# Performance work log

Hardware: AMD Instinct MI355X
Metric: run time of the kernel (lower is better)

## Reference

```python
import jax, jax.numpy as jnp
import numpy as np

N, L, H, D = 4, 1024, 8, 64

def setup_inputs() -> dict:
    key = jax.random.key(0)
    ks = jax.random.split(key, 6)
    names = ["q_real", "q_imag", "k_real", "k_imag", "v_real", "v_imag"]
    return {n: jax.random.normal(k, (N, L, H, D), dtype=jnp.float32) for n, k in zip(names, ks)}


def reference(q_real, q_imag, k_real, k_imag, v_real, v_imag):
    d = q_real.shape[-1]
    scale = 1.0 / np.sqrt(d).astype(np.float32)
    # complex QK^T: (ar+i*ai)(br+i*bi) -> 4 real einsums, scores shape (N,H,L,S)
    s_real = (jnp.einsum('nlhd,nshd->nhls', q_real, k_real)
              - jnp.einsum('nlhd,nshd->nhls', q_imag, k_imag))
    s_imag = (jnp.einsum('nlhd,nshd->nhls', q_real, k_imag)
              + jnp.einsum('nlhd,nshd->nhls', q_imag, k_real))
    # complex softmax = independent softmax on real and imag parts
    w_real = jax.nn.softmax(scale * s_real, axis=-1)
    w_imag = jax.nn.softmax(scale * s_imag, axis=-1)
    # complex_dropout on complex input is identity (original code drops nothing)
    # complex AV
    u_real = (jnp.einsum('nhls,nshd->nlhd', w_real, v_real)
              - jnp.einsum('nhls,nshd->nlhd', w_imag, v_imag))
    u_imag = (jnp.einsum('nhls,nshd->nlhd', w_real, v_imag)
              + jnp.einsum('nhls,nshd->nlhd', w_imag, v_real))
    # attn_weights.permute(0,2,1,3).mean(dim=-2): (N,H,L,S)->(N,L,H,S), mean over H -> (N,L,S)
    a_real = w_real.mean(axis=1)
    a_imag = w_imag.mean(axis=1)
    return (u_real, u_imag, a_real, a_imag)
```

## Files before the change

kernel.cpp:

```cpp
#include <hip/hip_runtime.h>

#define N_ 4
#define L_ 1024
#define H_ 8
#define D_ 64

typedef _Float16 f16x8 __attribute__((ext_vector_type(8)));
typedef _Float16 f16x4 __attribute__((ext_vector_type(4)));
typedef _Float16 f16x2 __attribute__((ext_vector_type(2)));
typedef float f32x4 __attribute__((ext_vector_type(4)));

#define MFMA(A, B, C) __builtin_amdgcn_mfma_f32_16x16x32_f16(A, B, C, 0, 0, 0)
#define EXP2(x) __builtin_amdgcn_exp2f(x)

__device__ __forceinline__ ushort f2h(float x) {
    union { _Float16 h; ushort u; } c;
    c.h = (_Float16)x;
    return c.u;
}
__device__ __forceinline__ f16x8 ld8(const ushort* p) {
    return *(const f16x8*)p;
}
__device__ __forceinline__ f16x4 pack4(float a, float b, float c, float d) {
    union { f16x4 v; f16x2 h[2]; } u;
    u.h[0] = __builtin_bit_cast(f16x2, __builtin_amdgcn_cvt_pkrtz(a, b));
    u.h[1] = __builtin_bit_cast(f16x2, __builtin_amdgcn_cvt_pkrtz(c, d));
    return u.v;
}
__device__ __forceinline__ f16x8 negf(f16x8 a) {
    uint4 u = __builtin_bit_cast(uint4, a);
    u.x ^= 0x80008000u; u.y ^= 0x80008000u; u.z ^= 0x80008000u; u.w ^= 0x80008000u;
    return __builtin_bit_cast(f16x8, u);
}
__device__ __forceinline__ f16x8 cvt8s(const float* p, float s) {
    float4 a = *(const float4*)p;
    float4 b = *(const float4*)(p + 4);
    union { f16x8 v; _Float16 e[8]; } u;
    u.e[0] = (_Float16)(a.x * s); u.e[1] = (_Float16)(a.y * s);
    u.e[2] = (_Float16)(a.z * s); u.e[3] = (_Float16)(a.w * s);
    u.e[4] = (_Float16)(b.x * s); u.e[5] = (_Float16)(b.y * s);
    u.e[6] = (_Float16)(b.z * s); u.e[7] = (_Float16)(b.w * s);
    return u.v;
}
#define SCQ 0.18033688011112f
__device__ __forceinline__ f16x8 cvt8(const float* p) { return cvt8s(p, SCQ); }

__device__ __forceinline__ void gl_lds16(const ushort* g, ushort* l) {
    __builtin_amdgcn_global_load_lds(
        (const __attribute__((address_space(1))) unsigned int*)g,
        (__attribute__((address_space(3))) unsigned int*)l, 16, 0, 0);
}

__global__ void cvt_kv(const float* __restrict__ k_r, const float* __restrict__ k_i,
                       const float* __restrict__ vr, const float* __restrict__ vi,
                       ushort* __restrict__ dst) {
    __shared__ ushort t[64][72];
    const int tid = threadIdx.x;
    if (blockIdx.x < 4096) {
        int gid = blockIdx.x * 256 + tid;
        int aid = gid >> 19;
        int idx = (gid & 0x7FFFF) << 2;
        int d  = idx & 63;
        int l  = (idx >> 6) & 1023;
        int hh = (idx >> 16) & 7;
        int n  = idx >> 19;
        const float* src = aid ? k_i : k_r;
        const float4 v = *(const float4*)(src + (((long)n * 1024 + l) * 8 + hh) * 64 + d);
        ushort4 o = make_ushort4(f2h(v.x), f2h(v.y), f2h(v.z), f2h(v.w));
        *(ushort4*)(dst + ((long)aid << 21) + idx) = o;
        return;
    }
    int bid = blockIdx.x - 4096;
    int aid = bid >> 9;
    int b   = bid & 511;
    int s0  = (b & 15) << 6;
    int hh  = (b >> 4) & 7;
    int n   = b >> 7;
    const float* src = aid ? vi : vr;
    int r  = tid >> 4;
    int cq = (tid & 15) << 2;
#pragma unroll
    for (int it = 0; it < 4; ++it) {
        int s = s0 + it * 16 + r;
        const float4 v = *(const float4*)(src + (((long)n * 1024 + s) * 8 + hh) * 64 + cq);
        t[it * 16 + r][cq + 0] = f2h(v.x);
        t[it * 16 + r][cq + 1] = f2h(v.y);
        t[it * 16 + r][cq + 2] = f2h(v.z);
        t[it * 16 + r][cq + 3] = f2h(v.w);
    }
    __syncthreads();
    const int rem = cq & 31;
    const int noff = (cq & 32) + (((rem & 15) >> 2) << 3) + ((rem >> 4) << 2);
#pragma unroll
    for (int it = 0; it < 4; ++it) {
        int dd = it * 16 + r;
        ushort4 o;
        o.x = t[cq + 0][dd]; o.y = t[cq + 1][dd]; o.z = t[cq + 2][dd]; o.w = t[cq + 3][dd];
        *(ushort4*)(dst + (2l << 21) + ((long)aid << 21) +
                    (((long)n * 8 + hh) * 64 + dd) * 1024 + s0 + noff) = o;
    }
}


__launch_bounds__(512, 4)
__global__ void attn_u(const float* __restrict__ qr_g, const float* __restrict__ qi_g,
                       const ushort* __restrict__ ws, float* __restrict__ rdbuf,
                       float* __restrict__ out) {
    __shared__ ushort stgK[2][4096];
    __shared__ ushort stgV[2][4096];

    const int tid  = threadIdx.x;
    const int lane = tid & 63;
    const int wv   = tid >> 6;
    const int p    = wv >> 2;
    const int lsub = wv & 3;
    const int col  = lane & 15;
    const int g    = lane >> 4;

    const int id = blockIdx.x;
    const int x  = id & 7;
    const int j  = id >> 3;
    const int nh = x * 4 + (j >> 4);
    const int n  = nh >> 3;
    const int h  = nh & 7;
    const int l0 = (j & 15) * 64 + lsub * 16;

    const ushort* Kr = ws + ((long)nh << 16);
    const ushort* Ki = ws + (1l << 21) + ((long)nh << 16);
    const ushort* Vr = ws + (2l << 21) + ((long)nh << 16);
    const ushort* Vi = ws + (3l << 21) + ((long)nh << 16);

    const long qg = (((long)n * 1024 + l0 + col) * 8 + h) * 64 + g * 8;
    const float sgn = p ? SCQ : -SCQ;
    const f16x8 qr0 = cvt8(qr_g + qg), qr1 = cvt8(qr_g + qg + 32);
    const f16x8 qx0 = cvt8s(qi_g + qg, sgn), qx1 = cvt8s(qi_g + qg + 32, sgn);

    const int kpart = tid >> 8;
    const int ksr   = (tid >> 3) & 31;
    const int kbo   = (tid & 7) ^ (ksr & 7);
    const ushort* Ksrc = (kpart ? Ki : Kr);
    const int vd  = tid >> 3;
    const int vb  = (tid & 7) ^ (vd & 7);
    const ushort* Vsrc = ((vb >> 2) ? Vi : Vr);
    const int vbo = (vb & 3) * 8;
    ushort* kdst0 = &stgK[0][wv * 512];
    ushort* kdst1 = &stgK[1][wv * 512];
    ushort* vdst0 = &stgV[0][wv * 512];
    ushort* vdst1 = &stgV[1][wv * 512];

    float dsum = 0.f;
    f32x4 uA[4], uB[4];
#pragma unroll
    for (int db = 0; db < 4; ++db) {
        uA[db] = (f32x4){0.f, 0.f, 0.f, 0.f};
        uB[db] = (f32x4){0.f, 0.f, 0.f, 0.f};
    }

    const int kx  = (g ^ (col & 7)) * 8;
    const int kx2 = ((g + 4) ^ (col & 7)) * 8;
    const int vxA = (g ^ (col & 7)) * 8;
    const int vxB = ((4 + g) ^ (col & 7)) * 8;

#define STAGE(kd, vd_, cc)                                                   \
    do {                                                                     \
        gl_lds16(Ksrc + (long)((cc) * 32 + ksr) * 64 + kbo * 8, kd);         \
        gl_lds16(Vsrc + (long)vd * 1024 + (cc) * 32 + vbo, vd_);             \
    } while (0)

    STAGE(kdst0, vdst0, 0);
    __syncthreads();

    for (int cc = 0; cc < 32; ++cc) {
        const int buf = cc & 1;
        if (cc < 31) {
            if (buf) STAGE(kdst0, vdst0, cc + 1);
            else     STAGE(kdst1, vdst1, cc + 1);
        }
        const ushort* sk = stgK[buf];
        const ushort* sv = stgV[buf];

        union { f16x8 w8; f16x4 q[2]; } pw;
#pragma unroll
        for (int sb = 0; sb < 2; ++sb) {
            const int rb = (sb * 16 + col) * 64;
            f16x8 ka0 = ld8(&sk[p * 2048 + rb + kx]);
            f16x8 ka1 = ld8(&sk[p * 2048 + rb + kx2]);
            f16x8 kb0 = ld8(&sk[(p ^ 1) * 2048 + rb + kx]);
            f16x8 kb1 = ld8(&sk[(p ^ 1) * 2048 + rb + kx2]);
            f32x4 a0 = (f32x4){0.f, 0.f, 0.f, 0.f};
            a0 = MFMA(ka0, qr0, a0); a0 = MFMA(ka1, qr1, a0);
            a0 = MFMA(kb0, qx0, a0); a0 = MFMA(kb1, qx1, a0);
            const float w0 = EXP2(a0[0]), w1 = EXP2(a0[1]);
            const float w2 = EXP2(a0[2]), w3 = EXP2(a0[3]);
            dsum += (w0 + w1) + (w2 + w3);
            pw.q[sb] = pack4(w0, w1, w2, w3);
        }

        __builtin_amdgcn_s_setprio(1);
#pragma unroll
        for (int db = 0; db < 4; ++db) {
            const int rv = (db * 16 + col) * 64;
            uA[db] = MFMA(pw.w8, ld8(&sv[rv + vxA]), uA[db]);
            uB[db] = MFMA(pw.w8, ld8(&sv[rv + vxB]), uB[db]);
        }
        __builtin_amdgcn_s_setprio(0);

        __syncthreads();
    }

    dsum += __shfl_xor(dsum, 16);
    dsum += __shfl_xor(dsum, 32);
    const float rd = 1.f / dsum;
    if (lane < 16) rdbuf[p * 32768 + nh * 1024 + l0 + col] = rd;

    float rdl[4];
#pragma unroll
    for (int r = 0; r < 4; ++r) rdl[r] = __shfl(rd, 4 * g + r);

#pragma unroll
    for (int db = 0; db < 4; ++db) {
#pragma unroll
        for (int r = 0; r < 4; ++r) {
            uA[db][r] *= rdl[r];
            uB[db][r] *= rdl[r];
        }
    }

    float* cb = (float*)&stgK[0][0];
    const int ci = (lsub * 64 + lane) * 16;
    if (p == 1) {
#pragma unroll
        for (int db = 0; db < 4; ++db) *(f32x4*)&cb[ci + db * 4] = uB[db];
    }
    __syncthreads();
    f32x4 oR[4];
    if (p == 0) {
#pragma unroll
        for (int db = 0; db < 4; ++db) oR[db] = uA[db] - *(f32x4*)&cb[ci + db * 4];
    }
    __syncthreads();
    if (p == 1) {
#pragma unroll
        for (int db = 0; db < 4; ++db) *(f32x4*)&cb[ci + db * 4] = uA[db];
    }
    __syncthreads();

    if (p == 0) {
        const long OFF_UI = 2097152;
#pragma unroll
        for (int db = 0; db < 4; ++db) {
            f32x4 oI = uB[db] + *(f32x4*)&cb[ci + db * 4];
#pragma unroll
            for (int r = 0; r < 4; ++r) {
                const int l = l0 + 4 * g + r;
                const int d = db * 16 + col;
                const long base = (((long)n * L_ + l) * H_ + h) * D_ + d;
                out[base] = oR[db][r];
                out[OFF_UI + base] = oI[r];
            }
        }
    }
#undef STAGE
}

__launch_bounds__(256, 4)
__global__ void kern_a(const float* __restrict__ qr_g, const float* __restrict__ qi_g,
                      const ushort* __restrict__ ws, const float* __restrict__ rdbuf,
                      float* __restrict__ out) {
    __shared__ ushort stgK[2][2][64][64];
    __shared__ float lrd[8][2][64];

    const int tid  = threadIdx.x;
    const int lane = tid & 63;
    const int wv   = tid >> 6;
    const int col  = lane & 15;
    const int g    = lane >> 4;

    const int id  = blockIdx.x;
    const int x   = id & 7;
    const int q   = id >> 3;
    const int n   = x >> 1;
    const int idx = (x & 1) * 128 + q;
    const int lt0 = (idx >> 4) * 64;
    const int sc  = idx & 15;
    const int l0  = lt0 + wv * 16;

    const ushort* KrB = ws + ((long)(n * 8) << 16);
    const ushort* KiB = ws + (1l << 21) + ((long)(n * 8) << 16);

#pragma unroll
    for (int i = 0; i < 4; ++i) {
        const int t = i * 256 + tid;
        (&lrd[0][0][0])[t] =
            rdbuf[((t >> 6) & 1) * 32768 + (n * 8 + (t >> 7)) * 1024 + lt0 + (t & 63)];
    }

    const int sp   = wv >> 1;
    const int kbs  = ((lane & 7) ^ (lane >> 3)) * 8;

#define STAGEA(buf, hh)                                                      \
    do {                                                                     \
        const ushort* Kp = (sp ? KiB : KrB) + ((long)(hh) << 16);            \
        _Pragma("unroll")                                                    \
        for (int i = 0; i < 4; ++i) {                                        \
            const int krow = (wv & 1) * 32 + i * 8 + (lane >> 3);            \
            gl_lds16(Kp + (long)(sc * 64 + krow) * 64 + kbs,                 \
                     &stgK[buf][sp][(wv & 1) * 32 + i * 8][0]);              \
        }                                                                    \
    } while (0)

    f32x4 aR[4], aI[4];
#pragma unroll
    for (int i = 0; i < 4; ++i) {
        aR[i] = (f32x4){0.f, 0.f, 0.f, 0.f};
        aI[i] = (f32x4){0.f, 0.f, 0.f, 0.f};
    }

    const int kx  = (g ^ (col & 7)) * 8;
    const int kx2 = ((g + 4) ^ (col & 7)) * 8;

    STAGEA(0, 0);
    __syncthreads();

    for (int h = 0; h < 8; ++h) {
        const int buf = h & 1;
        if (h < 7) STAGEA(buf ^ 1, h + 1);

        const long qg = (((long)n * 1024 + l0 + col) * 8 + h) * 64 + g * 8;
        const f16x8 qr0 = cvt8(qr_g + qg), qr1 = cvt8(qr_g + qg + 32);
        const f16x8 qi0 = cvt8(qi_g + qg), qi1 = cvt8(qi_g + qg + 32);
        const f16x8 qn0 = negf(qi0), qn1 = negf(qi1);

        float rdR[4], rdI[4];
#pragma unroll
        for (int r = 0; r < 4; ++r) {
            rdR[r] = lrd[h][0][wv * 16 + 4 * g + r];
            rdI[r] = lrd[h][1][wv * 16 + 4 * g + r];
        }

#pragma unroll
        for (int sb = 0; sb < 4; ++sb) {
            const int row = sb * 16 + col;
            f16x8 kr0 = ld8(&stgK[buf][0][row][kx]);
            f16x8 kr1 = ld8(&stgK[buf][0][row][kx2]);
            f16x8 ki0 = ld8(&stgK[buf][1][row][kx]);
            f16x8 ki1 = ld8(&stgK[buf][1][row][kx2]);
            f32x4 a0 = (f32x4){0.f, 0.f, 0.f, 0.f};
            a0 = MFMA(qr0, kr0, a0); a0 = MFMA(qr1, kr1, a0);
            a0 = MFMA(qn0, ki0, a0); a0 = MFMA(qn1, ki1, a0);
            f32x4 a1 = (f32x4){0.f, 0.f, 0.f, 0.f};
            a1 = MFMA(qr0, ki0, a1); a1 = MFMA(qr1, ki1, a1);
            a1 = MFMA(qi0, kr0, a1); a1 = MFMA(qi1, kr1, a1);
#pragma unroll
            for (int r = 0; r < 4; ++r) {
                aR[sb][r] += EXP2(a0[r]) * rdR[r];
                aI[sb][r] += EXP2(a1[r]) * rdI[r];
            }
        }
        __syncthreads();
    }

    const long OFF_AR = 4194304;
    const long OFF_AI = 8388608;
#pragma unroll
    for (int sb = 0; sb < 4; ++sb) {
#pragma unroll
        for (int r = 0; r < 4; ++r) {
            const int l = l0 + 4 * g + r;
            const int s = sc * 64 + sb * 16 + col;
            const long ab = ((long)n * 1024 + l) * 1024 + s;
            out[OFF_AR + ab] = aR[sb][r] * 0.125f;
            out[OFF_AI + ab] = aI[sb][r] * 0.125f;
        }
    }
#undef STAGEA
}

extern "C" void kernel_launch(void* const* d_in, const int* in_sizes, int n_in,
                              void* d_out, int out_size, void* d_ws, size_t ws_size,
                              hipStream_t stream) {
    const float* qr = (const float*)d_in[0];
    const float* qi = (const float*)d_in[1];
    const float* kr = (const float*)d_in[2];
    const float* ki = (const float*)d_in[3];
    const float* vr = (const float*)d_in[4];
    const float* vi = (const float*)d_in[5];
    ushort* ws = (ushort*)d_ws;
    float* rdbuf = (float*)((char*)d_ws + (16ull << 20));
    float* out = (float*)d_out;

    hipLaunchKernelGGL(cvt_kv, dim3(5120), dim3(256), 0, stream, kr, ki, vr, vi, ws);
    hipLaunchKernelGGL(attn_u, dim3(512), dim3(512), 0, stream, qr, qi, ws, rdbuf, out);
    hipLaunchKernelGGL(kern_a, dim3(1024), dim3(256), 0, stream, qr, qi, ws, rdbuf, out);
}
```

Before: 94.42 us.

## Halve attn_u block size to 256 threads with 32 query rows per block

Splits the attention-output kernel into 1024 blocks of 256 threads (4 waves), each covering 32 query rows instead of 64. Each thread now issues two K and two V global-to-LDS loads per stage to fill the same double-buffered tiles, and the final barrier is skipped. The aim is finer-grained scheduling and more resident blocks per CU. The cost is that each K/V tile is reused across fewer query rows, so more K/V traffic goes through L2 per unit of work.

```diff
diff --git a/kernel.cpp b/kernel.cpp
--- a/kernel.cpp
+++ b/kernel.cpp
@@ -102,7 +102,7 @@
 }
 
 
-__launch_bounds__(512, 4)
+__launch_bounds__(256, 5)
 __global__ void attn_u(const float* __restrict__ qr_g, const float* __restrict__ qi_g,
                        const ushort* __restrict__ ws, float* __restrict__ rdbuf,
                        float* __restrict__ out) {
@@ -112,18 +112,18 @@
     const int tid  = threadIdx.x;
     const int lane = tid & 63;
     const int wv   = tid >> 6;
-    const int p    = wv >> 2;
-    const int lsub = wv & 3;
+    const int p    = wv >> 1;
+    const int lsub = wv & 1;
     const int col  = lane & 15;
     const int g    = lane >> 4;
 
     const int id = blockIdx.x;
     const int x  = id & 7;
     const int j  = id >> 3;
-    const int nh = x * 4 + (j >> 4);
+    const int nh = x * 4 + (j >> 5);
     const int n  = nh >> 3;
     const int h  = nh & 7;
-    const int l0 = (j & 15) * 64 + lsub * 16;
+    const int l0 = (j & 31) * 32 + lsub * 16;
 
     const ushort* Kr = ws + ((long)nh << 16);
     const ushort* Ki = ws + (1l << 21) + ((long)nh << 16);
@@ -135,18 +135,18 @@
     const f16x8 qr0 = cvt8(qr_g + qg), qr1 = cvt8(qr_g + qg + 32);
     const f16x8 qx0 = cvt8s(qi_g + qg, sgn), qx1 = cvt8s(qi_g + qg + 32, sgn);
 
-    const int kpart = tid >> 8;
-    const int ksr   = (tid >> 3) & 31;
-    const int kbo   = (tid & 7) ^ (ksr & 7);
-    const ushort* Ksrc = (kpart ? Ki : Kr);
-    const int vd  = tid >> 3;
-    const int vb  = (tid & 7) ^ (vd & 7);
-    const ushort* Vsrc = ((vb >> 2) ? Vi : Vr);
-    const int vbo = (vb & 3) * 8;
-    ushort* kdst0 = &stgK[0][wv * 512];
-    ushort* kdst1 = &stgK[1][wv * 512];
-    ushort* vdst0 = &stgV[0][wv * 512];
-    ushort* vdst1 = &stgV[1][wv * 512];
+    const int ksr = (tid >> 3) & 31;
+    const int kbo = (tid & 7) ^ (ksr & 7);
+    const int vdA = tid >> 3;
+    const int vbA = (tid & 7) ^ (vdA & 7);
+    const ushort* VsA = ((vbA >> 2) ? Vi : Vr);
+    const int voA = (vbA & 3) * 8;
+    const int vdB = 32 + (tid >> 3);
+    const int vbB = (tid & 7) ^ (vdB & 7);
+    const ushort* VsB = ((vbB >> 2) ? Vi : Vr);
+    const int voB = (vbB & 3) * 8;
+    ushort* kbase = &stgK[0][wv * 512];
+    ushort* vbase = &stgV[0][wv * 512];
 
     float dsum = 0.f;
     f32x4 uA[4], uB[4];
@@ -161,21 +161,24 @@
     const int vxA = (g ^ (col & 7)) * 8;
     const int vxB = ((4 + g) ^ (col & 7)) * 8;
 
-#define STAGE(kd, vd_, cc)                                                   \
+#define STAGE(bb, cc)                                                        \
     do {                                                                     \
-        gl_lds16(Ksrc + (long)((cc) * 32 + ksr) * 64 + kbo * 8, kd);         \
-        gl_lds16(Vsrc + (long)vd * 1024 + (cc) * 32 + vbo, vd_);             \
+        gl_lds16(Kr + (long)((cc) * 32 + ksr) * 64 + kbo * 8,                \
+                 kbase + (bb) * 4096);                                       \
+        gl_lds16(Ki + (long)((cc) * 32 + ksr) * 64 + kbo * 8,                \
+                 kbase + (bb) * 4096 + 2048);                                \
+        gl_lds16(VsA + (long)vdA * 1024 + (cc) * 32 + voA,                   \
+                 vbase + (bb) * 4096);                                       \
+        gl_lds16(VsB + (long)vdB * 1024 + (cc) * 32 + voB,                   \
+                 vbase + (bb) * 4096 + 2048);                                \
     } while (0)
 
-    STAGE(kdst0, vdst0, 0);
+    STAGE(0, 0);
     __syncthreads();
 
     for (int cc = 0; cc < 32; ++cc) {
         const int buf = cc & 1;
-        if (cc < 31) {
-            if (buf) STAGE(kdst0, vdst0, cc + 1);
-            else     STAGE(kdst1, vdst1, cc + 1);
-        }
+        if (cc < 31) STAGE(buf ^ 1, cc + 1);
         const ushort* sk = stgK[buf];
         const ushort* sv = stgV[buf];
 
@@ -205,7 +208,8 @@
         }
         __builtin_amdgcn_s_setprio(0);
 
-        __syncthreads();
+        if (cc < 31) __syncthreads();
+        else break;
     }
 
     dsum += __shfl_xor(dsum, 16);
@@ -390,6 +394,6 @@
     float* out = (float*)d_out;
 
     hipLaunchKernelGGL(cvt_kv, dim3(5120), dim3(256), 0, stream, kr, ki, vr, vi, ws);
-    hipLaunchKernelGGL(attn_u, dim3(512), dim3(512), 0, stream, qr, qi, ws, rdbuf, out);
+    hipLaunchKernelGGL(attn_u, dim3(1024), dim3(256), 0, stream, qr, qi, ws, rdbuf, out);
     hipLaunchKernelGGL(kern_a, dim3(1024), dim3(256), 0, stream, qr, qi, ws, rdbuf, out);
 }
```

New measurement: 99.67 us. +5.6%, slower.
